# Optimization experiments

Hardware: AMD Instinct MI355X
Metric: run time of the kernel (lower is better)

The kernel has to match this reference:

```python
import jax, jax.numpy as jnp
import numpy as np

B, S, D, H = 2, 2048, 2048, 16
Dh = D // H


def _rotate_interleaved(t):
    # t: (..., Dh); pairs (x0,x1) -> (-x1, x0), interleaved
    t2 = t.reshape(t.shape[:-1] + (Dh // 2, 2))
    rot = jnp.stack([-t2[..., 1], t2[..., 0]], axis=-1)
    return rot.reshape(t.shape)


def _apply_rope(t, cos, sin):
    # t: (B,H,S,Dh); cos/sin: (S,Dh) broadcast over batch and heads
    return t * cos[None, None, :, :] + _rotate_interleaved(t) * sin[None, None, :, :]


def setup_inputs() -> dict:
    key = jax.random.key(0)
    ks = jax.random.split(key, 4)
    x = jax.random.normal(ks[0], (B, S, D), dtype=jnp.float32)
    wq = jax.random.normal(ks[1], (D, D), dtype=jnp.float32) * (D ** -0.5)
    wk = jax.random.normal(ks[2], (D, D), dtype=jnp.float32) * (D ** -0.5)
    wv = jax.random.normal(ks[3], (D, D), dtype=jnp.float32) * (D ** -0.5)
    # Real RoPE cos/sin tables: theta_i = 10000^{-2i/Dh}, interleaved layout
    inv_freq = 1.0 / (10000.0 ** (np.arange(0, Dh, 2, dtype=np.float32) / Dh))
    angles = np.arange(S, dtype=np.float32)[:, None] * inv_freq[None, :]  # (S, Dh/2)
    angles = np.repeat(angles, 2, axis=-1)  # (S, Dh) interleaved
    rope_cos = jnp.asarray(np.cos(angles))
    rope_sin = jnp.asarray(np.sin(angles))
    return {"x": x, "wq": wq, "wk": wk, "wv": wv,
            "rope_cos": rope_cos, "rope_sin": rope_sin}


def reference(x, wq, wk, wv, rope_cos, rope_sin):
    b, s, d = x.shape
    # QKV projections (torch Linear: y = x @ W^T), split into heads -> (B,H,S,Dh)
    def proj(w):
        return (x @ w.T).reshape(b, s, H, Dh).transpose(0, 2, 1, 3)
    q, k, v = proj(wq), proj(wk), proj(wv)
    cos, sin = rope_cos[:s], rope_sin[:s]
    q = _apply_rope(q, cos, sin)
    k = _apply_rope(k, cos, sin)
    # causal SDPA
    scores = jnp.einsum('bhqd,bhkd->bhqk', q, k) / jnp.sqrt(jnp.float32(Dh))
    causal = jnp.tril(jnp.ones((s, s), dtype=bool))
    scores = jnp.where(causal[None, None], scores, jnp.float32(-1e30))
    attn = jax.nn.softmax(scores, axis=-1)
    out = jnp.einsum('bhqk,bhkd->bhqd', attn, v)  # (B,H,S,Dh)
    # extra trailing softmax over head dim (as in source)
    out = jax.nn.softmax(out.astype(jnp.float32), axis=-1)
    return out.transpose(0, 2, 1, 3).reshape(b, s, -1)
```

## Files before the change

kernel.cpp:

```cpp
#include <hip/hip_runtime.h>

#define Bc 2
#define Sc 2048
#define Dc 2048
#define Hc 16
#define DHc 128

typedef _Float16 f16;
typedef __attribute__((ext_vector_type(4))) _Float16 v4h;
typedef __attribute__((ext_vector_type(8))) _Float16 v8h;
typedef __attribute__((ext_vector_type(4))) float v4f;
typedef __attribute__((ext_vector_type(16))) float v16f;
typedef __attribute__((ext_vector_type(4))) float f32x4;

__global__ void cvt_kernel(const float* __restrict__ x, const float* __restrict__ wq,
                           const float* __restrict__ wk, const float* __restrict__ wv,
                           f16* __restrict__ xh, f16* __restrict__ wqh,
                           f16* __restrict__ wkh, f16* __restrict__ wvh)
{
    int bid = blockIdx.x;
    const float* src; f16* dst; int idx;
    if (bid < 8192)       { src = x;  dst = xh;  idx = bid; }
    else if (bid < 12288) { src = wq; dst = wqh; idx = bid - 8192; }
    else if (bid < 16384) { src = wk; dst = wkh; idx = bid - 12288; }
    else                  { src = wv; dst = wvh; idx = bid - 16384; }
    int i = idx * 256 + threadIdx.x;
    f32x4 v = ((const f32x4*)src)[i];
    v4h hv; hv[0]=(f16)v[0]; hv[1]=(f16)v[1]; hv[2]=(f16)v[2]; hv[3]=(f16)v[3];
    ((v4h*)dst)[i] = hv;
}

__launch_bounds__(512, 2)
__global__ void proj256_kernel(const f16* __restrict__ xh, const f16* __restrict__ wall,
                               const float* __restrict__ cs, const float* __restrict__ sn,
                               f16* __restrict__ qh, f16* __restrict__ kh,
                               f16* __restrict__ vt)
{
    const int bid = blockIdx.x;
    const int swz = (bid & 7) * 96 + (bid >> 3);
    const int mt = swz & 31, nt = swz >> 5;
    const int m0 = mt * 128, n0 = nt * 256;

    const int tid = threadIdx.x;
    const int wid = tid >> 6, lane = tid & 63;
    const int wr = wid >> 2, wc = wid & 3;
    const int l15 = lane & 15, quad = lane >> 4;
    const int x7 = l15 & 7;

    __shared__ __align__(16) f16 lds[73728];

    const f16* aS[2]; const f16* bS[4];
    #pragma unroll
    for (int j = 0; j < 2; ++j) {
        int c = tid + j * 512;
        int r = c >> 3, s = c & 7;
        aS[j] = xh + (size_t)(m0 + r) * Dc + ((s ^ (r & 7)) * 8);
    }
    #pragma unroll
    for (int j = 0; j < 4; ++j) {
        int c = tid + j * 512;
        int r = c >> 3, s = c & 7;
        bS[j] = wall + (size_t)(n0 + r) * Dc + ((s ^ (r & 7)) * 8);
    }

#define GLD(src_, dst_)                                                         \
    __builtin_amdgcn_global_load_lds(                                           \
        (const __attribute__((address_space(1))) void*)(src_),                  \
        (__attribute__((address_space(3))) void*)(dst_), 16, 0, 0)

#define STAGE_P0(kt_, buf_) do {                                                \
        const int _ko = (kt_) * 64;                                             \
        f16* _b = lds + (buf_) * 24576;                                         \
        GLD(aS[0] + _ko, _b + wid * 512);                                       \
        GLD(aS[1] + _ko, _b + 4096 + wid * 512);                                \
        GLD(bS[0] + _ko, _b + 8192 + wid * 512);                                \
    } while (0)

#define STAGE_P1(kt_, buf_) do {                                                \
        const int _ko = (kt_) * 64;                                             \
        f16* _b = lds + (buf_) * 24576;                                         \
        GLD(bS[1] + _ko, _b + 8192 + 4096  + wid * 512);                        \
        GLD(bS[2] + _ko, _b + 8192 + 8192  + wid * 512);                        \
        GLD(bS[3] + _ko, _b + 8192 + 12288 + wid * 512);                        \
    } while (0)

#define VMW6  asm volatile("s_waitcnt vmcnt(6)"  ::: "memory")
#define VMW0  asm volatile("s_waitcnt vmcnt(0)"  ::: "memory")
#define LGKM0 asm volatile("s_waitcnt lgkmcnt(0)" ::: "memory")
#define BAR   __builtin_amdgcn_s_barrier()

#define PHASE(kk_, bR_) do {                                                    \
        const f16* _Ab = lds + (bR_) * 24576;                                   \
        const f16* _Bb = _Ab + 8192;                                            \
        v8h af[4], bf[4];                                                       \
        _Pragma("unroll")                                                       \
        for (int mi = 0; mi < 4; ++mi)                                          \
            af[mi] = *(const v8h*)(_Ab + (wr * 64 + mi * 16 + l15) * 64         \
                                   + ((((kk_) * 4 + quad) ^ x7) * 8));          \
        _Pragma("unroll")                                                       \
        for (int ni = 0; ni < 4; ++ni)                                          \
            bf[ni] = *(const v8h*)(_Bb + (wc * 64 + ni * 16 + l15) * 64         \
                                   + ((((kk_) * 4 + quad) ^ x7) * 8));          \
        PH_TAIL;                                                                \
        __builtin_amdgcn_s_setprio(1);                                          \
        _Pragma("unroll")                                                       \
        for (int mi = 0; mi < 4; ++mi)                                          \
            _Pragma("unroll")                                                   \
            for (int ni = 0; ni < 4; ++ni)                                      \
                acc[mi][ni] = __builtin_amdgcn_mfma_f32_16x16x32_f16(           \
                    af[mi], bf[ni], acc[mi][ni], 0, 0, 0);                      \
        __builtin_amdgcn_s_setprio(0);                                          \
    } while (0)

    v4f acc[4][4];
    #pragma unroll
    for (int i = 0; i < 4; ++i)
        #pragma unroll
        for (int j = 0; j < 4; ++j)
            acc[i][j] = (v4f){0.f, 0.f, 0.f, 0.f};

    STAGE_P0(0, 0); STAGE_P1(0, 0);
    STAGE_P0(1, 1); STAGE_P1(1, 1);
    VMW6;
    BAR;

    int bR = 0;
    int bSt = 2;

    #pragma unroll 1
    for (int t = 0; t < 32; ++t) {
        {
#define PH_TAIL do { if (t + 2 < 32) STAGE_P0(t + 2, bSt); BAR; } while (0)
            PHASE(0, bR);
#undef PH_TAIL
        }
        BAR;
        {
#define PH_TAIL do { if (t + 2 < 32) STAGE_P1(t + 2, bSt);                      \
                     if (t < 30) { VMW6; } else { VMW0; }                       \
                     BAR; } while (0)
            PHASE(1, bR);
#undef PH_TAIL
        }
        LGKM0;
        BAR;

        bR  = (bR  == 2) ? 0 : bR  + 1;
        bSt = (bSt == 2) ? 0 : bSt + 1;
    }

#undef STAGE_P0
#undef STAGE_P1
#undef GLD
#undef VMW6
#undef VMW0
#undef LGKM0
#undef BAR
#undef PHASE

    const int z = n0 >> 11;
    const int bb = m0 >> 11, s0 = m0 & 2047;

    if (z < 2) {
        f16 (*Ep)[264] = (f16(*)[264])lds;
        #pragma unroll
        for (int mi = 0; mi < 4; ++mi)
            #pragma unroll
            for (int ni = 0; ni < 4; ++ni)
                #pragma unroll
                for (int r = 0; r < 4; ++r)
                    Ep[wr * 64 + mi * 16 + quad * 4 + r][wc * 64 + ni * 16 + l15] =
                        (f16)acc[mi][ni][r];
        __syncthreads();
        f16* outp = (z == 0) ? qh : kh;
        const float scl = (z == 0) ? 0.08838834764831845f : 1.0f;
        #pragma unroll
        for (int it = 0; it < 8; ++it) {
            int ch = tid + it * 512, row = ch >> 5, c = ch & 31;
            v8h val = *(const v8h*)&Ep[row][c * 8];
            int s = s0 + row;
            int nn = (n0 & 2047) + c * 8;
            int h = nn >> 7, d0 = nn & 127;
            const float* cp = cs + (size_t)s * DHc + d0;
            const float* sp = sn + (size_t)s * DHc + d0;
            f32x4 ca = *(const f32x4*)cp, cb = *(const f32x4*)(cp + 4);
            f32x4 sa = *(const f32x4*)sp, sb = *(const f32x4*)(sp + 4);
            float v[8];
            #pragma unroll
            for (int j = 0; j < 8; ++j) v[j] = (float)val[j];
            v8h rv;
            rv[0] = (f16)((v[0]*ca[0] - v[1]*sa[0]) * scl);
            rv[1] = (f16)((v[1]*ca[1] + v[0]*sa[1]) * scl);
            rv[2] = (f16)((v[2]*ca[2] - v[3]*sa[2]) * scl);
            rv[3] = (f16)((v[3]*ca[3] + v[2]*sa[3]) * scl);
            rv[4] = (f16)((v[4]*cb[0] - v[5]*sb[0]) * scl);
            rv[5] = (f16)((v[5]*cb[1] + v[4]*sb[1]) * scl);
            rv[6] = (f16)((v[6]*cb[2] - v[7]*sb[2]) * scl);
            rv[7] = (f16)((v[7]*cb[3] + v[6]*sb[3]) * scl);
            *(v8h*)(outp + ((size_t)(bb * Hc + h) * Sc + s) * DHc + d0) = rv;
        }
    } else {
        f16 (*Ep)[136] = (f16(*)[136])lds;
        #pragma unroll
        for (int mi = 0; mi < 4; ++mi)
            #pragma unroll
            for (int ni = 0; ni < 4; ++ni)
                #pragma unroll
                for (int r = 0; r < 4; ++r)
                    Ep[wc * 64 + ni * 16 + l15][wr * 64 + mi * 16 + quad * 4 + r] =
                        (f16)acc[mi][ni][r];
        __syncthreads();
        #pragma unroll
        for (int it = 0; it < 8; ++it) {
            int ch = tid + it * 512, n = ch >> 4, cm = ch & 15;
            int nn = (n0 & 2047) + n;
            int h = nn >> 7, d = nn & 127;
            int s = s0 + cm * 8;
            *(v8h*)(vt + ((size_t)(bb * Hc + h) * DHc + d) * Sc + s) =
                *(const v8h*)&Ep[n][cm * 8];
        }
    }
}

__launch_bounds__(256)
__global__ void proj_kernel(const float* __restrict__ x, const float* __restrict__ wq,
                            const float* __restrict__ wk, const float* __restrict__ wv,
                            f16* __restrict__ qh, f16* __restrict__ kh, f16* __restrict__ vt)
{
    const int z = blockIdx.z;
    const float* w = (z == 0) ? wq : ((z == 1) ? wk : wv);
    const int m0 = blockIdx.x * 128, n0 = blockIdx.y * 128;
    const int tid = threadIdx.x, lane = tid & 63, wid = tid >> 6;
    const int wm = wid >> 1, wn = wid & 1;
    const int l15 = lane & 15, quad = lane >> 4;

    __shared__ __align__(16) f16 smem[2 * 128 * 72];
    f16 (*As)[72] = (f16(*)[72])smem;
    f16 (*Bs)[72] = (f16(*)[72])(smem + 128 * 72);

    v4f acc[4][4];
    for (int i = 0; i < 4; ++i)
        for (int j = 0; j < 4; ++j)
            acc[i][j] = (v4f){0.f, 0.f, 0.f, 0.f};

    for (int k0 = 0; k0 < Dc; k0 += 64) {
        __syncthreads();
        for (int it = 0; it < 4; ++it) {
            int chunk = tid + it * 256;
            int r = chunk >> 3, cc = chunk & 7;
            const f32x4* pa = (const f32x4*)(x + (size_t)(m0 + r) * Dc + k0 + cc * 8);
            f32x4 a0 = pa[0], a1 = pa[1];
            v8h ha;
            ha[0]=(f16)a0[0]; ha[1]=(f16)a0[1]; ha[2]=(f16)a0[2]; ha[3]=(f16)a0[3];
            ha[4]=(f16)a1[0]; ha[5]=(f16)a1[1]; ha[6]=(f16)a1[2]; ha[7]=(f16)a1[3];
            *(v8h*)&As[r][cc * 8] = ha;
            const f32x4* pb = (const f32x4*)(w + (size_t)(n0 + r) * Dc + k0 + cc * 8);
            f32x4 b0 = pb[0], b1 = pb[1];
            v8h hb;
            hb[0]=(f16)b0[0]; hb[1]=(f16)b0[1]; hb[2]=(f16)b0[2]; hb[3]=(f16)b0[3];
            hb[4]=(f16)b1[0]; hb[5]=(f16)b1[1]; hb[6]=(f16)b1[2]; hb[7]=(f16)b1[3];
            *(v8h*)&Bs[r][cc * 8] = hb;
        }
        __syncthreads();
        for (int kk = 0; kk < 2; ++kk) {
            v8h af[4], bf[4];
            for (int mi = 0; mi < 4; ++mi)
                af[mi] = *(const v8h*)&As[wm * 64 + mi * 16 + l15][kk * 32 + quad * 8];
            for (int ni = 0; ni < 4; ++ni)
                bf[ni] = *(const v8h*)&Bs[wn * 64 + ni * 16 + l15][kk * 32 + quad * 8];
            for (int mi = 0; mi < 4; ++mi)
                for (int ni = 0; ni < 4; ++ni)
                    acc[mi][ni] = __builtin_amdgcn_mfma_f32_16x16x32_f16(
                        af[mi], bf[ni], acc[mi][ni], 0, 0, 0);
        }
    }
    __syncthreads();
    f16 (*Ep)[136] = (f16(*)[136])smem;
    for (int mi = 0; mi < 4; ++mi)
        for (int ni = 0; ni < 4; ++ni)
            for (int r = 0; r < 4; ++r) {
                int ml = wm * 64 + mi * 16 + quad * 4 + r;
                int nl = wn * 64 + ni * 16 + l15;
                f16 val = (f16)acc[mi][ni][r];
                if (z == 2) Ep[nl][ml] = val;
                else        Ep[ml][nl] = val;
            }
    __syncthreads();
    const int b = m0 >> 11, s0 = m0 & 2047, h = n0 >> 7;
    if (z < 2) {
        f16* outp = (z == 0) ? qh : kh;
        for (int it = 0; it < 8; ++it) {
            int ch = tid + it * 256, row = ch >> 4, c = ch & 15;
            *(v8h*)(outp + ((size_t)((b * Hc + h) * Sc) + s0 + row) * DHc + c * 8) =
                *(const v8h*)&Ep[row][c * 8];
        }
    } else {
        for (int it = 0; it < 8; ++it) {
            int ch = tid + it * 256, row = ch >> 4, c = ch & 15;
            *(v8h*)(vt + ((size_t)((b * Hc + h) * DHc) + row) * Sc + s0 + c * 8) =
                *(const v8h*)&Ep[row][c * 8];
        }
    }
}

__global__ void rope_kernel(f16* __restrict__ qh, f16* __restrict__ kh,
                            const float* __restrict__ cs, const float* __restrict__ sn)
{
    int i  = blockIdx.x * 256 + threadIdx.x;
    int d2 = i & 63;
    int s  = (i >> 6) & (Sc - 1);
    int bh = i >> 17;
    f16* t = blockIdx.y ? kh : qh;
    float scale = blockIdx.y ? 1.0f : 0.08838834764831845f;
    float c  = cs[s * DHc + 2 * d2];
    float sv = sn[s * DHc + 2 * d2];
    f16* p = t + ((size_t)bh * Sc + s) * DHc + 2 * d2;
    float t0 = (float)p[0], t1 = (float)p[1];
    p[0] = (f16)((t0 * c - t1 * sv) * scale);
    p[1] = (f16)((t1 * c + t0 * sv) * scale);
}

__launch_bounds__(512, 2)
__global__ void attn_kernel(const f16* __restrict__ qh, const f16* __restrict__ kh,
                            const f16* __restrict__ vt, float* __restrict__ out)
{
    const int L = blockIdx.x;
    const int slot = L >> 3;
    const int bh = (L & 7) * 4 + (slot >> 3);
    const int p  = slot & 7;
    const int b = bh >> 4, h = bh & 15;
    const int tid = threadIdx.x, lane = tid & 63, w = tid >> 6;
    const int g = w >> 2, wg = w & 3;
    const int l31 = lane & 31, half = lane >> 5;
    const int sw = l31 & 7;

    __shared__ __align__(16) f16 smem[32768];
    f16* ksm = smem;
    f16* vsm = smem + 16384;

    const size_t bhoff = (size_t)bh * Sc * DHc;

    const f16* ksrc[2]; const f16* vsrc[2];
    f16* kdst[2]; f16* vdst[2];
    #pragma unroll
    for (int j = 0; j < 2; ++j) {
        int slot0 = j * 512 + w * 64;
        {   int r = (slot0 >> 4) + (lane >> 4);
            int c = (lane & 15) ^ (r & 7);
            ksrc[j] = kh + bhoff + (size_t)r * DHc + c * 8;
            kdst[j] = ksm + slot0 * 8; }
        {   int r = (slot0 >> 3) + (lane >> 3);
            int c = (lane & 7) ^ (r & 7);
            vsrc[j] = vt + bhoff + (size_t)r * Sc + c * 8;
            vdst[j] = vsm + slot0 * 8; }
    }

#define STAGE(kt_, buf_) do {                                                   \
        int _ko = (kt_) * 64 * DHc;                                             \
        int _vo = (kt_) * 64;                                                   \
        int _lb = (buf_) * 8192;                                                \
        _Pragma("unroll")                                                       \
        for (int j = 0; j < 2; ++j) {                                           \
            __builtin_amdgcn_global_load_lds(                                   \
                (const __attribute__((address_space(1))) void*)(ksrc[j] + _ko), \
                (__attribute__((address_space(3))) void*)(kdst[j] + _lb), 16, 0, 0); \
            __builtin_amdgcn_global_load_lds(                                   \
                (const __attribute__((address_space(1))) void*)(vsrc[j] + _vo), \
                (__attribute__((address_space(3))) void*)(vdst[j] + _lb), 16, 0, 0); \
        } } while (0)

    const int qt  = g ? p : 15 - p;
    const int nkt = 2 * (15 - p) + 2;
    const int q0  = qt * 128 + wg * 32;
    const int qg  = q0 + l31;

    v8h qf[8];
    const f16* qrow = qh + bhoff + (size_t)qg * DHc;
    #pragma unroll
    for (int s = 0; s < 8; ++s)
        qf[s] = *(const v8h*)(qrow + s * 16 + half * 8);

    float l_run = 0.f;
    v16f o[4];
    #pragma unroll
    for (int i = 0; i < 4; ++i)
        #pragma unroll
        for (int r = 0; r < 16; ++r) o[i][r] = 0.f;

    STAGE(0, 0);

    #pragma unroll 1
    for (int kt = 0; kt < nkt; ++kt) {
        __syncthreads();
        if (kt + 1 < nkt) STAGE(kt + 1, (kt + 1) & 1);
        if (q0 + 31 < kt * 64) continue;

        const f16* kbuf = ksm + (kt & 1) * 8192;
        const f16* vbuf = vsm + (kt & 1) * 8192;
        const bool do1 = (kt * 64 + 32 <= q0 + 31);

        v16f st0, st1;
        #pragma unroll
        for (int r = 0; r < 16; ++r) { st0[r] = 0.f; st1[r] = 0.f; }
        #pragma unroll
        for (int s = 0; s < 8; ++s) {
            int c = ((s * 2 + half) ^ sw) * 8;
            v8h kf0 = *(const v8h*)(kbuf + l31 * 128 + c);
            st0 = __builtin_amdgcn_mfma_f32_32x32x16_f16(kf0, qf[s], st0, 0, 0, 0);
            if (do1) {
                v8h kf1 = *(const v8h*)(kbuf + (32 + l31) * 128 + c);
                st1 = __builtin_amdgcn_mfma_f32_32x32x16_f16(kf1, qf[s], st1, 0, 0, 0);
            }
        }

        float sum = 0.f;
        #pragma unroll
        for (int r = 0; r < 16; ++r) {
            int key = kt * 64 + (r & 3) + 8 * (r >> 2) + 4 * half;
            float sv = (key > qg) ? -1e30f : st0[r];
            float pe = __expf(sv);
            st0[r] = pe; sum += pe;
        }
        if (do1) {
            #pragma unroll
            for (int r = 0; r < 16; ++r) {
                int key = kt * 64 + 32 + (r & 3) + 8 * (r >> 2) + 4 * half;
                float sv = (key > qg) ? -1e30f : st1[r];
                float pe = __expf(sv);
                st1[r] = pe; sum += pe;
            }
        }
        sum += __shfl_xor(sum, 32);
        l_run += sum;

        #pragma unroll
        for (int s2 = 0; s2 < 4; ++s2) {
            v4h bfr;
            bfr[0]=(f16)st0[4*s2]; bfr[1]=(f16)st0[4*s2+1];
            bfr[2]=(f16)st0[4*s2+2]; bfr[3]=(f16)st0[4*s2+3];
            int c = ((s2 ^ sw) * 8) + half * 4;
            #pragma unroll
            for (int dt = 0; dt < 4; ++dt) {
                v4h vf = *(const v4h*)(vbuf + (dt * 32 + l31) * 64 + c);
                o[dt] = __builtin_amdgcn_mfma_f32_32x32x8f16(vf, bfr, o[dt], 0, 0, 0);
            }
        }
        if (do1) {
            #pragma unroll
            for (int s2 = 0; s2 < 4; ++s2) {
                v4h bfr;
                bfr[0]=(f16)st1[4*s2]; bfr[1]=(f16)st1[4*s2+1];
                bfr[2]=(f16)st1[4*s2+2]; bfr[3]=(f16)st1[4*s2+3];
                int c = (((4 + s2) ^ sw) * 8) + half * 4;
                #pragma unroll
                for (int dt = 0; dt < 4; ++dt) {
                    v4h vf = *(const v4h*)(vbuf + (dt * 32 + l31) * 64 + c);
                    o[dt] = __builtin_amdgcn_mfma_f32_32x32x8f16(vf, bfr, o[dt], 0, 0, 0);
                }
            }
        }
    }

    float inv = 1.f / l_run;
    float mxd = -1e30f;
    #pragma unroll
    for (int dt = 0; dt < 4; ++dt)
        #pragma unroll
        for (int r = 0; r < 16; ++r) {
            o[dt][r] *= inv;
            mxd = fmaxf(mxd, o[dt][r]);
        }
    mxd = fmaxf(mxd, __shfl_xor(mxd, 32));
    float sd = 0.f;
    #pragma unroll
    for (int dt = 0; dt < 4; ++dt)
        #pragma unroll
        for (int r = 0; r < 16; ++r) {
            float t = __expf(o[dt][r] - mxd);
            o[dt][r] = t;
            sd += t;
        }
    sd += __shfl_xor(sd, 32);
    float rinv = 1.f / sd;

    float* orow = out + (size_t)(b * Sc + qg) * Dc + h * DHc;
    #pragma unroll
    for (int dt = 0; dt < 4; ++dt)
        #pragma unroll
        for (int g2 = 0; g2 < 4; ++g2) {
            f32x4 vv;
            vv[0] = o[dt][4*g2+0] * rinv;
            vv[1] = o[dt][4*g2+1] * rinv;
            vv[2] = o[dt][4*g2+2] * rinv;
            vv[3] = o[dt][4*g2+3] * rinv;
            *(f32x4*)(orow + dt * 32 + g2 * 8 + half * 4) = vv;
        }
#undef STAGE
}

extern "C" void kernel_launch(void* const* d_in, const int* in_sizes, int n_in,
                              void* d_out, int out_size, void* d_ws, size_t ws_size,
                              hipStream_t stream)
{
    const float* x  = (const float*)d_in[0];
    const float* wq = (const float*)d_in[1];
    const float* wk = (const float*)d_in[2];
    const float* wv = (const float*)d_in[3];
    const float* cs = (const float*)d_in[4];
    const float* sn = (const float*)d_in[5];
    float* out = (float*)d_out;

    const size_t tsz = (size_t)Bc * Hc * Sc * DHc;
    f16* qh = (f16*)d_ws;
    f16* kh = qh + tsz;
    f16* vt = kh + tsz;

    if (ws_size >= 11 * tsz) {
        f16* xh  = vt + tsz;
        f16* wqh = xh + tsz;
        f16* wkh = wqh + tsz / 2;
        f16* wvh = wkh + tsz / 2;
        cvt_kernel<<<20480, 256, 0, stream>>>(x, wq, wk, wv, xh, wqh, wkh, wvh);
        proj256_kernel<<<768, 512, 0, stream>>>(xh, wqh, cs, sn, qh, kh, vt);
    } else {
        proj_kernel<<<dim3(32, 16, 3), 256, 0, stream>>>(x, wq, wk, wv, qh, kh, vt);
        rope_kernel<<<dim3(16384, 2), 256, 0, stream>>>(qh, kh, cs, sn);
    }
    attn_kernel<<<256, 512, 0, stream>>>(qh, kh, vt, out);
}
```

Baseline: 306.7 us.

## Split causal KV range between warp groups with per-group LDS and merge

Each of the two 4-wave groups in a block now streams its own K/V tiles into a separate LDS region. Both groups run a fixed 17-iteration loop. Group 1 first finishes the short (early) query tile, writes its output, then processes the tail key tiles of the long query tile. Group 0 processes the leading key tiles of the long tile. Group 1's partial accumulators and row sums are then passed through LDS and added in by group 0 before the final normalization and head-dim softmax. This balances the causal work between groups, which previously shared every key tile up to the long tile's length. In exchange, LDS use per block doubles, which likely limits occupancy to one block per CU, and global K/V traffic is duplicated across the two groups.

New measurement: 297.5 us. 3.0% less time.

```diff
diff --git a/kernel.cpp b/kernel.cpp
--- a/kernel.cpp
+++ b/kernel.cpp
@@ -330,21 +330,22 @@
     const int p  = slot & 7;
     const int b = bh >> 4, h = bh & 15;
     const int tid = threadIdx.x, lane = tid & 63, w = tid >> 6;
-    const int g = w >> 2, wg = w & 3;
+    const int grp = w >> 2, wg = w & 3;
     const int l31 = lane & 31, half = lane >> 5;
     const int sw = l31 & 7;
 
-    __shared__ __align__(16) f16 smem[32768];
-    f16* ksm = smem;
-    f16* vsm = smem + 16384;
+    __shared__ __align__(16) f16 smem[65536];
+    f16* gbase = smem + grp * 32768;
+    f16* ksm = gbase;
+    f16* vsm = gbase + 16384;
 
     const size_t bhoff = (size_t)bh * Sc * DHc;
 
-    const f16* ksrc[2]; const f16* vsrc[2];
-    f16* kdst[2]; f16* vdst[2];
+    const f16* ksrc[4]; const f16* vsrc[4];
+    f16* kdst[4]; f16* vdst[4];
     #pragma unroll
-    for (int j = 0; j < 2; ++j) {
-        int slot0 = j * 512 + w * 64;
+    for (int j = 0; j < 4; ++j) {
+        int slot0 = j * 256 + wg * 64;
         {   int r = (slot0 >> 4) + (lane >> 4);
             int c = (lane & 15) ^ (r & 7);
             ksrc[j] = kh + bhoff + (size_t)r * DHc + c * 8;
@@ -360,7 +361,7 @@
         int _vo = (kt_) * 64;                                                   \
         int _lb = (buf_) * 8192;                                                \
         _Pragma("unroll")                                                       \
-        for (int j = 0; j < 2; ++j) {                                           \
+        for (int j = 0; j < 4; ++j) {                                           \
             __builtin_amdgcn_global_load_lds(                                   \
                 (const __attribute__((address_space(1))) void*)(ksrc[j] + _ko), \
                 (__attribute__((address_space(3))) void*)(kdst[j] + _lb), 16, 0, 0); \
@@ -369,16 +370,56 @@
                 (__attribute__((address_space(3))) void*)(vdst[j] + _lb), 16, 0, 0); \
         } } while (0)
 
-    const int qt  = g ? p : 15 - p;
-    const int nkt = 2 * (15 - p) + 2;
-    const int q0  = qt * 128 + wg * 32;
-    const int qg  = q0 + l31;
+#define EPILOG do {                                                             \
+        float inv = 1.f / l_run;                                               \
+        float mxd = -1e30f;                                                    \
+        _Pragma("unroll")                                                      \
+        for (int dt = 0; dt < 4; ++dt)                                         \
+            _Pragma("unroll")                                                  \
+            for (int r = 0; r < 16; ++r) {                                     \
+                o[dt][r] *= inv;                                               \
+                mxd = fmaxf(mxd, o[dt][r]);                                    \
+            }                                                                  \
+        mxd = fmaxf(mxd, __shfl_xor(mxd, 32));                                 \
+        float sd = 0.f;                                                        \
+        _Pragma("unroll")                                                      \
+        for (int dt = 0; dt < 4; ++dt)                                         \
+            _Pragma("unroll")                                                  \
+            for (int r = 0; r < 16; ++r) {                                     \
+                float tv = __expf(o[dt][r] - mxd);                             \
+                o[dt][r] = tv;                                                 \
+                sd += tv;                                                      \
+            }                                                                  \
+        sd += __shfl_xor(sd, 32);                                              \
+        float rinv = 1.f / sd;                                                 \
+        float* orow = out + (size_t)(b * Sc + qg) * Dc + h * DHc;              \
+        _Pragma("unroll")                                                      \
+        for (int dt = 0; dt < 4; ++dt)                                         \
+            _Pragma("unroll")                                                  \
+            for (int g2 = 0; g2 < 4; ++g2) {                                   \
+                f32x4 vv;                                                      \
+                vv[0] = o[dt][4*g2+0] * rinv;                                  \
+                vv[1] = o[dt][4*g2+1] * rinv;                                  \
+                vv[2] = o[dt][4*g2+2] * rinv;                                  \
+                vv[3] = o[dt][4*g2+3] * rinv;                                  \
+                *(f32x4*)(orow + dt * 32 + g2 * 8 + half * 4) = vv;            \
+            }                                                                  \
+    } while (0)
+
+    const int tp_end = 2 * p + 2;
+    const int tailoff = 15 - 2 * p;
+
+    int qt = grp ? p : (15 - p);
+    int q0 = qt * 128 + wg * 32;
+    int qg = q0 + l31;
 
     v8h qf[8];
-    const f16* qrow = qh + bhoff + (size_t)qg * DHc;
-    #pragma unroll
-    for (int s = 0; s < 8; ++s)
-        qf[s] = *(const v8h*)(qrow + s * 16 + half * 8);
+    {
+        const f16* qrow = qh + bhoff + (size_t)qg * DHc;
+        #pragma unroll
+        for (int s = 0; s < 8; ++s)
+            qf[s] = *(const v8h*)(qrow + s * 16 + half * 8);
+    }
 
     float l_run = 0.f;
     v16f o[4];
@@ -390,14 +431,32 @@
     STAGE(0, 0);
 
     #pragma unroll 1
-    for (int kt = 0; kt < nkt; ++kt) {
+    for (int i = 0; i < 17; ++i) {
         __syncthreads();
-        if (kt + 1 < nkt) STAGE(kt + 1, (kt + 1) & 1);
-        if (q0 + 31 < kt * 64) continue;
-
-        const f16* kbuf = ksm + (kt & 1) * 8192;
-        const f16* vbuf = vsm + (kt & 1) * 8192;
-        const bool do1 = (kt * 64 + 32 <= q0 + 31);
+        if (i < 16) {
+            int inx = i + 1;
+            int kn = (grp == 0) ? inx : ((inx < tp_end) ? inx : inx + tailoff);
+            STAGE(kn, inx & 1);
+        }
+        if (grp == 1 && i == tp_end) {
+            EPILOG;
+            l_run = 0.f;
+            #pragma unroll
+            for (int d2 = 0; d2 < 4; ++d2)
+                #pragma unroll
+                for (int r = 0; r < 16; ++r) o[d2][r] = 0.f;
+            qt = 15 - p; q0 = qt * 128 + wg * 32; qg = q0 + l31;
+            const f16* qrow = qh + bhoff + (size_t)qg * DHc;
+            #pragma unroll
+            for (int s = 0; s < 8; ++s)
+                qf[s] = *(const v8h*)(qrow + s * 16 + half * 8);
+        }
+        const int kv = (grp == 0) ? i : ((i < tp_end) ? i : i + tailoff);
+        if (q0 + 31 < kv * 64) continue;
+
+        const f16* kbuf = ksm + (i & 1) * 8192;
+        const f16* vbuf = vsm + (i & 1) * 8192;
+        const bool do1 = (kv * 64 + 32 <= q0 + 31);
 
         v16f st0, st1;
         #pragma unroll
@@ -416,7 +475,7 @@
         float sum = 0.f;
         #pragma unroll
         for (int r = 0; r < 16; ++r) {
-            int key = kt * 64 + (r & 3) + 8 * (r >> 2) + 4 * half;
+            int key = kv * 64 + (r & 3) + 8 * (r >> 2) + 4 * half;
             float sv = (key > qg) ? -1e30f : st0[r];
             float pe = __expf(sv);
             st0[r] = pe; sum += pe;
@@ -424,7 +483,7 @@
         if (do1) {
             #pragma unroll
             for (int r = 0; r < 16; ++r) {
-                int key = kt * 64 + 32 + (r & 3) + 8 * (r >> 2) + 4 * half;
+                int key = kv * 64 + 32 + (r & 3) + 8 * (r >> 2) + 4 * half;
                 float sv = (key > qg) ? -1e30f : st1[r];
                 float pe = __expf(sv);
                 st1[r] = pe; sum += pe;
@@ -461,41 +520,29 @@
         }
     }
 
-    float inv = 1.f / l_run;
-    float mxd = -1e30f;
-    #pragma unroll
-    for (int dt = 0; dt < 4; ++dt)
-        #pragma unroll
-        for (int r = 0; r < 16; ++r) {
-            o[dt][r] *= inv;
-            mxd = fmaxf(mxd, o[dt][r]);
-        }
-    mxd = fmaxf(mxd, __shfl_xor(mxd, 32));
-    float sd = 0.f;
-    #pragma unroll
-    for (int dt = 0; dt < 4; ++dt)
-        #pragma unroll
-        for (int r = 0; r < 16; ++r) {
-            float t = __expf(o[dt][r] - mxd);
-            o[dt][r] = t;
-            sd += t;
-        }
-    sd += __shfl_xor(sd, 32);
-    float rinv = 1.f / sd;
-
-    float* orow = out + (size_t)(b * Sc + qg) * Dc + h * DHc;
-    #pragma unroll
-    for (int dt = 0; dt < 4; ++dt)
-        #pragma unroll
-        for (int g2 = 0; g2 < 4; ++g2) {
-            f32x4 vv;
-            vv[0] = o[dt][4*g2+0] * rinv;
-            vv[1] = o[dt][4*g2+1] * rinv;
-            vv[2] = o[dt][4*g2+2] * rinv;
-            vv[3] = o[dt][4*g2+3] * rinv;
-            *(f32x4*)(orow + dt * 32 + g2 * 8 + half * 4) = vv;
-        }
+    __syncthreads();
+    float* ox = (float*)smem;
+    float* lx = (float*)smem + 16384;
+    if (grp == 1) {
+        #pragma unroll
+        for (int dt = 0; dt < 4; ++dt)
+            #pragma unroll
+            for (int r = 0; r < 16; ++r)
+                ox[wg * 4096 + (dt * 16 + r) * 64 + lane] = o[dt][r];
+        lx[wg * 64 + lane] = l_run;
+    }
+    __syncthreads();
+    if (grp == 0) {
+        #pragma unroll
+        for (int dt = 0; dt < 4; ++dt)
+            #pragma unroll
+            for (int r = 0; r < 16; ++r)
+                o[dt][r] += ox[wg * 4096 + (dt * 16 + r) * 64 + lane];
+        l_run += lx[wg * 64 + lane];
+        EPILOG;
+    }
 #undef STAGE
+#undef EPILOG
 }
 
 extern "C" void kernel_launch(void* const* d_in, const int* in_sizes, int n_in,
```
